# Performance work log

Measured on AMD Instinct MI355X. Metric: run time of the kernel, lower is better.

Reference implementation:

```python
import jax, jax.numpy as jnp
import numpy as np

N = 100000      # num nodes
E = 1600000     # num edges (avg degree 16)
F_IN = 256      # num_node_features
HID = 128       # hid_dim
C = 16          # num_classes


def gcn_conv(x, W, b, src, dst, num_nodes):
    # Linear transform first (PyG GCNConv transforms then aggregates)
    h = x @ W  # [N, out]
    # Symmetric normalization with self-loops already included in src/dst
    ones = jnp.ones_like(dst, dtype=h.dtype)
    deg = jax.ops.segment_sum(ones, dst, num_segments=num_nodes)  # in-degree incl. self-loop
    dinv = jnp.where(deg > 0, jax.lax.rsqrt(deg), 0.0)
    norm = dinv[src] * dinv[dst]                 # [E+N]
    msg = h[src] * norm[:, None]                 # gather + scale
    out = jax.ops.segment_sum(msg, dst, num_segments=num_nodes)  # scatter-add
    return out + b


def setup_inputs() -> dict:
    key = jax.random.key(0)
    k = jax.random.split(key, 4)
    x = jax.random.normal(k[0], (N, F_IN), dtype=jnp.float32)
    edge_index = jax.random.randint(k[1], (2, E), 0, N, dtype=jnp.int32)
    W1 = jax.random.normal(k[2], (F_IN, HID), dtype=jnp.float32) * (1.0 / np.sqrt(F_IN))
    b1 = jnp.zeros((HID,), dtype=jnp.float32)
    W2 = jax.random.normal(k[3], (HID, C), dtype=jnp.float32) * (1.0 / np.sqrt(HID))
    b2 = jnp.zeros((C,), dtype=jnp.float32)
    return {"x": x, "edge_index": edge_index, "W1": W1, "b1": b1, "W2": W2, "b2": b2}


def reference(x, edge_index, W1, b1, W2, b2):
    num_nodes = x.shape[0]
    loop = jnp.arange(num_nodes, dtype=edge_index.dtype)
    src = jnp.concatenate([edge_index[0], loop])  # add self-loops
    dst = jnp.concatenate([edge_index[1], loop])
    h = gcn_conv(x, W1, b1, src, dst, num_nodes)
    h = jax.nn.relu(h)
    # F.dropout(training=self.training): identity in eval mode
    out = gcn_conv(h, W2, b2, src, dst, num_nodes)
    return out
```

## Files before the change

kernel.cpp:

```cpp
#include <hip/hip_runtime.h>
#include <cstddef>

#define CAP 48

typedef short short8 __attribute__((ext_vector_type(8)));
typedef float floatx4 __attribute__((ext_vector_type(4)));

__device__ inline float b2f_lo(unsigned int u) {
  union { unsigned int i; float f; } c;
  c.i = u << 16;
  return c.f;
}
__device__ inline float b2f_hi(unsigned int u) {
  union { unsigned int i; float f; } c;
  c.i = u & 0xFFFF0000u;
  return c.f;
}
__device__ inline unsigned short f2b(float f) {
  union { float f; unsigned int i; } c;
  c.f = f;
  unsigned int u = c.i;
  unsigned int r = (u + 0x7FFFu + ((u >> 16) & 1u)) >> 16;
  return (unsigned short)r;
}
__device__ inline float dinv_of(int c) { return rsqrtf((float)(c + 1)); }

__global__ void k_prep(int* __restrict__ cnt, int N,
                       const float* __restrict__ W1, unsigned short* __restrict__ W1T) {
  int i = blockIdx.x * 256 + threadIdx.x;
  if (i < N) cnt[i] = 0;
  if (i < 256 * 128) {
    int k = i >> 7, n = i & 127;
    W1T[n * 256 + k] = f2b(W1[i]);
  }
}

__global__ __launch_bounds__(256) void k_build_gemm1(
    const int* __restrict__ src, const int* __restrict__ dst, int E, int N,
    int* __restrict__ cnt, int* __restrict__ bucket,
    const float* __restrict__ X, const unsigned short* __restrict__ W1T,
    unsigned short* __restrict__ H1, int M, int gblocks, int total) {
  __shared__ unsigned short As[32 * 40];
  __shared__ unsigned short Bs[128 * 40];

  const unsigned int idx = blockIdx.x;
  const unsigned int gBefore = (idx * (unsigned int)gblocks) / (unsigned int)total;
  const unsigned int gAfter = ((idx + 1) * (unsigned int)gblocks) / (unsigned int)total;
  const bool isGemm = (gAfter > gBefore);

  if (!isGemm) {
    const int bi = (int)(idx - gBefore);
    const int tb = bi * 256 + (int)threadIdx.x;
    const int i0 = tb * 4;
    if (i0 >= E) return;
    if (i0 + 3 < E) {
      int4 d4 = *(const int4*)(dst + i0);
      int4 s4 = *(const int4*)(src + i0);
      int p0 = atomicAdd(&cnt[d4.x], 1);
      int p1 = atomicAdd(&cnt[d4.y], 1);
      int p2 = atomicAdd(&cnt[d4.z], 1);
      int p3 = atomicAdd(&cnt[d4.w], 1);
      if (p0 < CAP) bucket[(size_t)d4.x * CAP + p0] = s4.x;
      if (p1 < CAP) bucket[(size_t)d4.y * CAP + p1] = s4.y;
      if (p2 < CAP) bucket[(size_t)d4.z * CAP + p2] = s4.z;
      if (p3 < CAP) bucket[(size_t)d4.w * CAP + p3] = s4.w;
    } else {
      for (int i = i0; i < E; ++i) {
        int d = dst[i], s = src[i];
        int pos = atomicAdd(&cnt[d], 1);
        if (pos < CAP) bucket[(size_t)d * CAP + pos] = s;
      }
    }
    return;
  }

  const int bid = (int)gBefore;
  const int tid = threadIdx.x;
  const int wave = tid >> 6;
  const int lane = tid & 63;
  const int quad = lane >> 4;
  const int l16 = lane & 15;
  const int row0 = bid * 32;
  const int n0 = wave * 32;

  floatx4 acc[2][2];
#pragma unroll
  for (int r = 0; r < 2; r++)
#pragma unroll
    for (int c = 0; c < 2; c++) acc[r][c] = (floatx4){0.f, 0.f, 0.f, 0.f};

  for (int k0 = 0; k0 < 256; k0 += 32) {
    {
      int r = tid >> 3;
      int q = tid & 7;
      int gr = row0 + r;
      float4 v = make_float4(0.f, 0.f, 0.f, 0.f);
      if (gr < M) v = *(const float4*)(X + (size_t)gr * 256 + k0 + q * 4);
      unsigned short tmp[4];
      tmp[0] = f2b(v.x); tmp[1] = f2b(v.y); tmp[2] = f2b(v.z); tmp[3] = f2b(v.w);
      *(uint2*)(As + r * 40 + q * 4) = *(const uint2*)(tmp);
    }
    {
      int n = tid >> 1;
      int half = (tid & 1) * 16;
      const uint4* wp = (const uint4*)(W1T + (size_t)n * 256 + k0 + half);
      uint4 w0 = wp[0];
      uint4 w1 = wp[1];
      unsigned short* p = Bs + n * 40 + half;
      *(uint4*)(p) = w0;
      *(uint4*)(p + 8) = w1;
    }
    __syncthreads();

    short8 afr[2], bfr[2];
#pragma unroll
    for (int r = 0; r < 2; r++)
      afr[r] = *(const short8*)(As + (r * 16 + l16) * 40 + quad * 8);
#pragma unroll
    for (int c = 0; c < 2; c++)
      bfr[c] = *(const short8*)(Bs + (n0 + c * 16 + l16) * 40 + quad * 8);
#pragma unroll
    for (int r = 0; r < 2; r++)
#pragma unroll
      for (int c = 0; c < 2; c++)
        acc[r][c] = __builtin_amdgcn_mfma_f32_16x16x32_bf16(afr[r], bfr[c], acc[r][c], 0, 0, 0);
    __syncthreads();
  }

#pragma unroll
  for (int r = 0; r < 2; r++) {
#pragma unroll
    for (int c = 0; c < 2; c++) {
      int col = n0 + c * 16 + l16;
#pragma unroll
      for (int i = 0; i < 4; i++) {
        int gr = row0 + r * 16 + quad * 4 + i;
        if (gr < M) H1[(size_t)gr * 128 + col] = f2b(acc[r][c][i]);
      }
    }
  }
}

__global__ __launch_bounds__(256) void k_agg1g2(const unsigned short* __restrict__ H1,
                                                const int* __restrict__ cnt,
                                                const int* __restrict__ bucket,
                                                const float* __restrict__ b1,
                                                const float* __restrict__ W2,
                                                unsigned short* __restrict__ H2, int N) {
  __shared__ float Ws[16 * 130];
  {
    int t = threadIdx.x;
    if (t < 128) {
      const float4* s4 = (const float4*)(W2 + t * 16);
      float4 w0 = s4[0], w1 = s4[1], w2v = s4[2], w3 = s4[3];
      float* d = Ws + (t >> 3) * 130 + (t & 7) * 16;
      d[0] = w0.x;  d[1] = w0.y;  d[2] = w0.z;  d[3] = w0.w;
      d[4] = w1.x;  d[5] = w1.y;  d[6] = w1.z;  d[7] = w1.w;
      d[8] = w2v.x; d[9] = w2v.y; d[10] = w2v.z; d[11] = w2v.w;
      d[12] = w3.x; d[13] = w3.y; d[14] = w3.z; d[15] = w3.w;
    }
  }
  __syncthreads();

  const int lane = threadIdx.x & 15;
  const int node = blockIdx.x * 16 + (threadIdx.x >> 4);
  if (node >= N) return;
  const int cn = cnt[node];
  const float di = dinv_of(cn);
  const int deg = min(cn, CAP);
  const int* bk = bucket + (size_t)node * CAP;

  int idx0 = (lane < deg) ? bk[lane] : 0;
  int idx1 = (lane + 16 < deg) ? bk[lane + 16] : 0;
  int idx2 = (lane + 32 < deg) ? bk[lane + 32] : 0;
  float dv0 = (lane < deg) ? dinv_of(cnt[idx0]) : 0.f;
  float dv1 = (lane + 16 < deg) ? dinv_of(cnt[idx1]) : 0.f;
  float dv2 = (lane + 32 < deg) ? dinv_of(cnt[idx2]) : 0.f;

  uint4 hs = ((const uint4*)(H1 + (size_t)node * 128))[lane];
  float a0 = b2f_lo(hs.x) * di, a1 = b2f_hi(hs.x) * di;
  float a2 = b2f_lo(hs.y) * di, a3 = b2f_hi(hs.y) * di;
  float a4 = b2f_lo(hs.z) * di, a5 = b2f_hi(hs.z) * di;
  float a6 = b2f_lo(hs.w) * di, a7 = b2f_hi(hs.w) * di;
  float c0 = 0.f, c1 = 0.f, c2 = 0.f, c3 = 0.f, c4 = 0.f, c5 = 0.f, c6 = 0.f, c7 = 0.f;

  for (int j = 0; j < deg; j += 8) {
    int b = j >> 4;
    int idxB = (b == 0) ? idx0 : ((b == 1) ? idx1 : idx2);
    float dvB = (b == 0) ? dv0 : ((b == 1) ? dv1 : dv2);
    int base = j & 15;
    int s0 = __shfl(idxB, base + 0, 16);
    int s1 = __shfl(idxB, base + 1, 16);
    int s2 = __shfl(idxB, base + 2, 16);
    int s3 = __shfl(idxB, base + 3, 16);
    int s4 = __shfl(idxB, base + 4, 16);
    int s5 = __shfl(idxB, base + 5, 16);
    int s6 = __shfl(idxB, base + 6, 16);
    int s7 = __shfl(idxB, base + 7, 16);
    float w0 = __shfl(dvB, base + 0, 16);
    float w1 = __shfl(dvB, base + 1, 16);
    float w2 = __shfl(dvB, base + 2, 16);
    float w3 = __shfl(dvB, base + 3, 16);
    float w4 = __shfl(dvB, base + 4, 16);
    float w5 = __shfl(dvB, base + 5, 16);
    float w6 = __shfl(dvB, base + 6, 16);
    float w7 = __shfl(dvB, base + 7, 16);
    uint4 v0 = ((const uint4*)(H1 + (size_t)s0 * 128))[lane];
    uint4 v1 = ((const uint4*)(H1 + (size_t)s1 * 128))[lane];
    uint4 v2 = ((const uint4*)(H1 + (size_t)s2 * 128))[lane];
    uint4 v3 = ((const uint4*)(H1 + (size_t)s3 * 128))[lane];
    uint4 v4 = ((const uint4*)(H1 + (size_t)s4 * 128))[lane];
    uint4 v5 = ((const uint4*)(H1 + (size_t)s5 * 128))[lane];
    uint4 v6 = ((const uint4*)(H1 + (size_t)s6 * 128))[lane];
    uint4 v7 = ((const uint4*)(H1 + (size_t)s7 * 128))[lane];
    a0 += b2f_lo(v0.x) * w0; a1 += b2f_hi(v0.x) * w0;
    a2 += b2f_lo(v0.y) * w0; a3 += b2f_hi(v0.y) * w0;
    a4 += b2f_lo(v0.z) * w0; a5 += b2f_hi(v0.z) * w0;
    a6 += b2f_lo(v0.w) * w0; a7 += b2f_hi(v0.w) * w0;
    c0 += b2f_lo(v1.x) * w1; c1 += b2f_hi(v1.x) * w1;
    c2 += b2f_lo(v1.y) * w1; c3 += b2f_hi(v1.y) * w1;
    c4 += b2f_lo(v1.z) * w1; c5 += b2f_hi(v1.z) * w1;
    c6 += b2f_lo(v1.w) * w1; c7 += b2f_hi(v1.w) * w1;
    a0 += b2f_lo(v2.x) * w2; a1 += b2f_hi(v2.x) * w2;
    a2 += b2f_lo(v2.y) * w2; a3 += b2f_hi(v2.y) * w2;
    a4 += b2f_lo(v2.z) * w2; a5 += b2f_hi(v2.z) * w2;
    a6 += b2f_lo(v2.w) * w2; a7 += b2f_hi(v2.w) * w2;
    c0 += b2f_lo(v3.x) * w3; c1 += b2f_hi(v3.x) * w3;
    c2 += b2f_lo(v3.y) * w3; c3 += b2f_hi(v3.y) * w3;
    c4 += b2f_lo(v3.z) * w3; c5 += b2f_hi(v3.z) * w3;
    c6 += b2f_lo(v3.w) * w3; c7 += b2f_hi(v3.w) * w3;
    a0 += b2f_lo(v4.x) * w4; a1 += b2f_hi(v4.x) * w4;
    a2 += b2f_lo(v4.y) * w4; a3 += b2f_hi(v4.y) * w4;
    a4 += b2f_lo(v4.z) * w4; a5 += b2f_hi(v4.z) * w4;
    a6 += b2f_lo(v4.w) * w4; a7 += b2f_hi(v4.w) * w4;
    c0 += b2f_lo(v5.x) * w5; c1 += b2f_hi(v5.x) * w5;
    c2 += b2f_lo(v5.y) * w5; c3 += b2f_hi(v5.y) * w5;
    c4 += b2f_lo(v5.z) * w5; c5 += b2f_hi(v5.z) * w5;
    c6 += b2f_lo(v5.w) * w5; c7 += b2f_hi(v5.w) * w5;
    a0 += b2f_lo(v6.x) * w6; a1 += b2f_hi(v6.x) * w6;
    a2 += b2f_lo(v6.y) * w6; a3 += b2f_hi(v6.y) * w6;
    a4 += b2f_lo(v6.z) * w6; a5 += b2f_hi(v6.z) * w6;
    a6 += b2f_lo(v6.w) * w6; a7 += b2f_hi(v6.w) * w6;
    c0 += b2f_lo(v7.x) * w7; c1 += b2f_hi(v7.x) * w7;
    c2 += b2f_lo(v7.y) * w7; c3 += b2f_hi(v7.y) * w7;
    c4 += b2f_lo(v7.z) * w7; c5 += b2f_hi(v7.z) * w7;
    c6 += b2f_lo(v7.w) * w7; c7 += b2f_hi(v7.w) * w7;
  }
  a0 += c0; a1 += c1; a2 += c2; a3 += c3;
  a4 += c4; a5 += c5; a6 += c6; a7 += c7;

  float4 bb0 = ((const float4*)b1)[lane * 2];
  float4 bb1 = ((const float4*)b1)[lane * 2 + 1];
  float av[8];
  av[0] = fmaxf(fmaf(a0, di, bb0.x), 0.f); av[1] = fmaxf(fmaf(a1, di, bb0.y), 0.f);
  av[2] = fmaxf(fmaf(a2, di, bb0.z), 0.f); av[3] = fmaxf(fmaf(a3, di, bb0.w), 0.f);
  av[4] = fmaxf(fmaf(a4, di, bb1.x), 0.f); av[5] = fmaxf(fmaf(a5, di, bb1.y), 0.f);
  av[6] = fmaxf(fmaf(a6, di, bb1.z), 0.f); av[7] = fmaxf(fmaf(a7, di, bb1.w), 0.f);

  float2 p2[8];
#pragma unroll
  for (int c = 0; c < 8; c++) p2[c] = make_float2(0.f, 0.f);
  const float* wl = Ws + lane * 130;
#pragma unroll
  for (int i = 0; i < 8; i++) {
    const float a = av[i];
    const float2* wr = (const float2*)(wl + i * 16);
#pragma unroll
    for (int c = 0; c < 8; c++) {
      float2 wv = wr[c];
      p2[c].x += a * wv.x;
      p2[c].y += a * wv.y;
    }
  }
  float p[16];
#pragma unroll
  for (int c = 0; c < 8; c++) { p[2 * c] = p2[c].x; p[2 * c + 1] = p2[c].y; }

  float k8[8];
  {
    const bool hi = (lane & 8) != 0;
#pragma unroll
    for (int i = 0; i < 8; i++) {
      float keep = hi ? p[8 + i] : p[i];
      float send = hi ? p[i] : p[8 + i];
      k8[i] = keep + __shfl_xor(send, 8, 16);
    }
  }
  float k4[4];
  {
    const bool hi = (lane & 4) != 0;
#pragma unroll
    for (int i = 0; i < 4; i++) {
      float keep = hi ? k8[4 + i] : k8[i];
      float send = hi ? k8[i] : k8[4 + i];
      k4[i] = keep + __shfl_xor(send, 4, 16);
    }
  }
  float k2[2];
  {
    const bool hi = (lane & 2) != 0;
#pragma unroll
    for (int i = 0; i < 2; i++) {
      float keep = hi ? k4[2 + i] : k4[i];
      float send = hi ? k4[i] : k4[2 + i];
      k2[i] = keep + __shfl_xor(send, 2, 16);
    }
  }
  float v;
  {
    const bool hi = (lane & 1) != 0;
    float keep = hi ? k2[1] : k2[0];
    float send = hi ? k2[0] : k2[1];
    v = keep + __shfl_xor(send, 1, 16);
  }
  H2[(size_t)node * 16 + lane] = f2b(v * di);
}

__global__ __launch_bounds__(256) void k_agg2(const unsigned short* __restrict__ H2,
                                              const int* __restrict__ cnt,
                                              const int* __restrict__ bucket,
                                              const float* __restrict__ b2,
                                              float* __restrict__ out, int N) {
  const int t = threadIdx.x;
  const int half = t & 1;
  const int par = (t >> 1) & 1;
  const int node = blockIdx.x * 64 + (t >> 2);
  if (node >= N) return;
  const int cn = cnt[node];
  const float di = dinv_of(cn);
  const int deg = min(cn, CAP);
  const int* bk = bucket + (size_t)node * CAP;

  float a0 = 0.f, a1 = 0.f, a2 = 0.f, a3 = 0.f, a4 = 0.f, a5 = 0.f, a6 = 0.f, a7 = 0.f;
  if (par == 0) {
    uint4 h = ((const uint4*)(H2 + (size_t)node * 16))[half];
    a0 = b2f_lo(h.x); a1 = b2f_hi(h.x);
    a2 = b2f_lo(h.y); a3 = b2f_hi(h.y);
    a4 = b2f_lo(h.z); a5 = b2f_hi(h.z);
    a6 = b2f_lo(h.w); a7 = b2f_hi(h.w);
  }

  for (int j = par * 4; j < deg; j += 8) {
    int4 s4 = *(const int4*)(bk + j);
    int s0 = s4.x;
    int s1 = (j + 1 < deg) ? s4.y : 0;
    int s2 = (j + 2 < deg) ? s4.z : 0;
    int s3 = (j + 3 < deg) ? s4.w : 0;
    float m1 = (j + 1 < deg) ? 1.f : 0.f;
    float m2 = (j + 2 < deg) ? 1.f : 0.f;
    float m3 = (j + 3 < deg) ? 1.f : 0.f;
    uint4 v0 = ((const uint4*)(H2 + (size_t)s0 * 16))[half];
    uint4 v1 = ((const uint4*)(H2 + (size_t)s1 * 16))[half];
    uint4 v2 = ((const uint4*)(H2 + (size_t)s2 * 16))[half];
    uint4 v3 = ((const uint4*)(H2 + (size_t)s3 * 16))[half];
    a0 += b2f_lo(v0.x); a1 += b2f_hi(v0.x);
    a2 += b2f_lo(v0.y); a3 += b2f_hi(v0.y);
    a4 += b2f_lo(v0.z); a5 += b2f_hi(v0.z);
    a6 += b2f_lo(v0.w); a7 += b2f_hi(v0.w);
    a0 = fmaf(b2f_lo(v1.x), m1, a0); a1 = fmaf(b2f_hi(v1.x), m1, a1);
    a2 = fmaf(b2f_lo(v1.y), m1, a2); a3 = fmaf(b2f_hi(v1.y), m1, a3);
    a4 = fmaf(b2f_lo(v1.z), m1, a4); a5 = fmaf(b2f_hi(v1.z), m1, a5);
    a6 = fmaf(b2f_lo(v1.w), m1, a6); a7 = fmaf(b2f_hi(v1.w), m1, a7);
    a0 = fmaf(b2f_lo(v2.x), m2, a0); a1 = fmaf(b2f_hi(v2.x), m2, a1);
    a2 = fmaf(b2f_lo(v2.y), m2, a2); a3 = fmaf(b2f_hi(v2.y), m2, a3);
    a4 = fmaf(b2f_lo(v2.z), m2, a4); a5 = fmaf(b2f_hi(v2.z), m2, a5);
    a6 = fmaf(b2f_lo(v2.w), m2, a6); a7 = fmaf(b2f_hi(v2.w), m2, a7);
    a0 = fmaf(b2f_lo(v3.x), m3, a0); a1 = fmaf(b2f_hi(v3.x), m3, a1);
    a2 = fmaf(b2f_lo(v3.y), m3, a2); a3 = fmaf(b2f_hi(v3.y), m3, a3);
    a4 = fmaf(b2f_lo(v3.z), m3, a4); a5 = fmaf(b2f_hi(v3.z), m3, a5);
    a6 = fmaf(b2f_lo(v3.w), m3, a6); a7 = fmaf(b2f_hi(v3.w), m3, a7);
  }

  a0 += __shfl_xor(a0, 2); a1 += __shfl_xor(a1, 2);
  a2 += __shfl_xor(a2, 2); a3 += __shfl_xor(a3, 2);
  a4 += __shfl_xor(a4, 2); a5 += __shfl_xor(a5, 2);
  a6 += __shfl_xor(a6, 2); a7 += __shfl_xor(a7, 2);

  if (par == 0) {
    float4 bb0 = ((const float4*)b2)[half * 2];
    float4 bb1 = ((const float4*)b2)[half * 2 + 1];
    float4 o0 = make_float4(fmaf(a0, di, bb0.x), fmaf(a1, di, bb0.y),
                            fmaf(a2, di, bb0.z), fmaf(a3, di, bb0.w));
    float4 o1 = make_float4(fmaf(a4, di, bb1.x), fmaf(a5, di, bb1.y),
                            fmaf(a6, di, bb1.z), fmaf(a7, di, bb1.w));
    ((float4*)(out + (size_t)node * 16))[half * 2] = o0;
    ((float4*)(out + (size_t)node * 16))[half * 2 + 1] = o1;
  }
}


extern "C" void kernel_launch(void* const* d_in, const int* in_sizes, int n_in,
                              void* d_out, int out_size, void* d_ws, size_t ws_size,
                              hipStream_t stream) {
  const float* x  = (const float*)d_in[0];
  const int* eidx = (const int*)d_in[1];
  const float* W1 = (const float*)d_in[2];
  const float* b1 = (const float*)d_in[3];
  const float* W2 = (const float*)d_in[4];
  const float* b2 = (const float*)d_in[5];
  float* out = (float*)d_out;

  const int HID = in_sizes[3];
  const int F   = in_sizes[2] / HID;
  const int N   = in_sizes[0] / F;
  const int E   = in_sizes[1] / 2;
  (void)n_in; (void)out_size; (void)ws_size;

  const int* src = eidx;
  const int* dst = eidx + E;

  char* base = (char*)d_ws;
  size_t off = 0;
  auto alloc = [&](size_t bytes) -> char* {
    char* p = base + off;
    off = (off + bytes + 255) & ~(size_t)255;
    return p;
  };
  int*            cnt    = (int*)alloc((size_t)N * 4);
  int*            bucket = (int*)alloc((size_t)N * CAP * 4);
  unsigned short* w1t    = (unsigned short*)alloc((size_t)256 * 128 * 2);
  unsigned short* h1     = (unsigned short*)alloc((size_t)N * 128 * 2);
  unsigned short* h2     = (unsigned short*)alloc((size_t)N * 16 * 2);

  const int nbN = (N + 255) / 256;
  const int gblocks = (N + 31) / 32;
  const int quads = (E + 3) / 4;
  const int nbuild = (quads + 255) / 256;
  const int total = nbuild + gblocks;

  hipLaunchKernelGGL(k_prep, dim3(nbN), dim3(256), 0, stream, cnt, N, W1, w1t);
  hipLaunchKernelGGL(k_build_gemm1, dim3(total), dim3(256), 0, stream,
                     src, dst, E, N, cnt, bucket, x, w1t, h1, N, gblocks, total);
  hipLaunchKernelGGL(k_agg1g2, dim3((N + 15) / 16), dim3(256), 0, stream, h1, cnt, bucket,
                     b1, W2, h2, N);
  hipLaunchKernelGGL(k_agg2, dim3((N + 63) / 64), dim3(256), 0, stream, h2, cnt, bucket,
                     b2, out, N);
}
```

Baseline: 333.8 us.

## Load GEMM1 MFMA fragments directly from global memory, dropping LDS staging

The first-layer GEMM no longer stages X and W1T tiles in shared memory with barriers. Each wave now owns 16 rows and all 128 output columns. It loads its A fragment straight from X, converts it to bf16 in registers, and reads B fragments directly from the bf16 W1T in global memory (likely cache-resident). The block tile grows from 32 to 64 rows, which halves the GEMM block count. This removes LDS traffic and syncs, at the cost of redundant W1T global loads per wave and less coalesced X reads.

```diff
diff --git a/kernel.cpp b/kernel.cpp
--- a/kernel.cpp
+++ b/kernel.cpp
@@ -40,9 +40,6 @@
     int* __restrict__ cnt, int* __restrict__ bucket,
     const float* __restrict__ X, const unsigned short* __restrict__ W1T,
     unsigned short* __restrict__ H1, int M, int gblocks, int total) {
-  __shared__ unsigned short As[32 * 40];
-  __shared__ unsigned short Bs[128 * 40];
-
   const unsigned int idx = blockIdx.x;
   const unsigned int gBefore = (idx * (unsigned int)gblocks) / (unsigned int)total;
   const unsigned int gAfter = ((idx + 1) * (unsigned int)gblocks) / (unsigned int)total;
@@ -80,63 +77,37 @@
   const int lane = tid & 63;
   const int quad = lane >> 4;
   const int l16 = lane & 15;
-  const int row0 = bid * 32;
-  const int n0 = wave * 32;
-
-  floatx4 acc[2][2];
-#pragma unroll
-  for (int r = 0; r < 2; r++)
-#pragma unroll
-    for (int c = 0; c < 2; c++) acc[r][c] = (floatx4){0.f, 0.f, 0.f, 0.f};
+  const int row0 = bid * 64;
+
+  const int myrow = row0 + wave * 16 + l16;
+  const int ldrow = (myrow < M) ? myrow : 0;
+  const float* xr = X + (size_t)ldrow * 256 + quad * 8;
+
+  floatx4 acc[8];
+#pragma unroll
+  for (int c = 0; c < 8; c++) acc[c] = (floatx4){0.f, 0.f, 0.f, 0.f};
 
   for (int k0 = 0; k0 < 256; k0 += 32) {
-    {
-      int r = tid >> 3;
-      int q = tid & 7;
-      int gr = row0 + r;
-      float4 v = make_float4(0.f, 0.f, 0.f, 0.f);
-      if (gr < M) v = *(const float4*)(X + (size_t)gr * 256 + k0 + q * 4);
-      unsigned short tmp[4];
-      tmp[0] = f2b(v.x); tmp[1] = f2b(v.y); tmp[2] = f2b(v.z); tmp[3] = f2b(v.w);
-      *(uint2*)(As + r * 40 + q * 4) = *(const uint2*)(tmp);
-    }
-    {
-      int n = tid >> 1;
-      int half = (tid & 1) * 16;
-      const uint4* wp = (const uint4*)(W1T + (size_t)n * 256 + k0 + half);
-      uint4 w0 = wp[0];
-      uint4 w1 = wp[1];
-      unsigned short* p = Bs + n * 40 + half;
-      *(uint4*)(p) = w0;
-      *(uint4*)(p + 8) = w1;
-    }
-    __syncthreads();
-
-    short8 afr[2], bfr[2];
-#pragma unroll
-    for (int r = 0; r < 2; r++)
-      afr[r] = *(const short8*)(As + (r * 16 + l16) * 40 + quad * 8);
-#pragma unroll
-    for (int c = 0; c < 2; c++)
-      bfr[c] = *(const short8*)(Bs + (n0 + c * 16 + l16) * 40 + quad * 8);
-#pragma unroll
-    for (int r = 0; r < 2; r++)
-#pragma unroll
-      for (int c = 0; c < 2; c++)
-        acc[r][c] = __builtin_amdgcn_mfma_f32_16x16x32_bf16(afr[r], bfr[c], acc[r][c], 0, 0, 0);
-    __syncthreads();
-  }
-
-#pragma unroll
-  for (int r = 0; r < 2; r++) {
-#pragma unroll
-    for (int c = 0; c < 2; c++) {
-      int col = n0 + c * 16 + l16;
-#pragma unroll
-      for (int i = 0; i < 4; i++) {
-        int gr = row0 + r * 16 + quad * 4 + i;
-        if (gr < M) H1[(size_t)gr * 128 + col] = f2b(acc[r][c][i]);
-      }
+    float4 v0 = *(const float4*)(xr + k0);
+    float4 v1 = *(const float4*)(xr + k0 + 4);
+    union { unsigned short us[8]; short8 s8; } af;
+    af.us[0] = f2b(v0.x); af.us[1] = f2b(v0.y); af.us[2] = f2b(v0.z); af.us[3] = f2b(v0.w);
+    af.us[4] = f2b(v1.x); af.us[5] = f2b(v1.y); af.us[6] = f2b(v1.z); af.us[7] = f2b(v1.w);
+    const short8 afr = af.s8;
+#pragma unroll
+    for (int c = 0; c < 8; c++) {
+      short8 bfr = *(const short8*)(W1T + (size_t)(c * 16 + l16) * 256 + k0 + quad * 8);
+      acc[c] = __builtin_amdgcn_mfma_f32_16x16x32_bf16(afr, bfr, acc[c], 0, 0, 0);
+    }
+  }
+
+#pragma unroll
+  for (int c = 0; c < 8; c++) {
+    int col = c * 16 + l16;
+#pragma unroll
+    for (int i = 0; i < 4; i++) {
+      int gr = row0 + wave * 16 + quad * 4 + i;
+      if (gr < M) H1[(size_t)gr * 128 + col] = f2b(acc[c][i]);
     }
   }
 }
@@ -423,7 +394,7 @@
   unsigned short* h2     = (unsigned short*)alloc((size_t)N * 16 * 2);
 
   const int nbN = (N + 255) / 256;
-  const int gblocks = (N + 31) / 32;
+  const int gblocks = (N + 63) / 64;
   const int quads = (E + 3) / 4;
   const int nbuild = (quads + 255) / 256;
   const int total = nbuild + gblocks;
```

After: 395.7 us. 18.5% more time.
